# Performance work log

Measured on AMD Instinct MI355X. Metric: run time of the kernel, lower is better.

## Reference

```python
import jax, jax.numpy as jnp
import numpy as np

N = 1024
X_DIM = 128
Y_DIM = 128
HID = 256


def setup_inputs() -> dict:
    key = jax.random.key(0)
    ks = jax.random.split(key, 8)
    x_samples = jax.random.normal(ks[0], (N, X_DIM), dtype=jnp.float32)
    y_samples = jax.random.normal(ks[1], (N, Y_DIM), dtype=jnp.float32)
    # F_func: Linear(x_dim+y_dim -> hidden), ReLU, Linear(hidden -> 1)
    W1 = jax.random.normal(ks[2], (HID, X_DIM + Y_DIM), dtype=jnp.float32) * 0.05
    b1 = jax.random.normal(ks[3], (HID,), dtype=jnp.float32) * 0.05
    w2 = jax.random.normal(ks[4], (HID,), dtype=jnp.float32) * 0.05  # Linear(hidden,1) weight
    b2 = jax.random.normal(ks[5], (), dtype=jnp.float32) * 0.05
    # baseline: Linear(y_dim -> 1)
    wb = jax.random.normal(ks[6], (Y_DIM,), dtype=jnp.float32) * 0.05
    bb = jax.random.normal(ks[7], (), dtype=jnp.float32) * 0.05
    return {"x_samples": x_samples, "y_samples": y_samples,
            "W1": W1, "b1": b1, "w2": w2, "b2": b2, "wb": wb, "bb": bb}


def reference(x_samples, y_samples, W1, b1, w2, b2, wb, bb):
    n = y_samples.shape[0]
    # Split first linear: F(x,y) first layer = x @ Wx^T + y @ Wy^T + b1
    # (identical math to Linear on concat([x, y]))
    Wx = W1[:, :X_DIM]  # [H, x_dim]
    Wy = W1[:, X_DIM:]  # [H, y_dim]
    px = x_samples @ Wx.T  # [N, H]
    py = y_samples @ Wy.T  # [N, H]

    # T0: F on paired samples (x_i, y_i) -> [N]
    T0 = jax.nn.relu(px + py + b1) @ w2 + b2

    # T1[i, j] = F(x_j, y_i): x tiled over dim 0, y tiled over dim 1
    h = jax.nn.relu(px[None, :, :] + py[:, None, :] + b1)  # [N, N, H]
    T1 = h @ w2 + b2  # [N, N]

    # baseline log-scores on y -> [N]
    log_scores = y_samples @ wb + bb

    # (T1 - log_scores) broadcasts log_scores along dim 1 (the j/x axis),
    # matching torch's [N,N,1] - [N,1] broadcast; logsumexp over dim 1.
    lse = jax.scipy.special.logsumexp(T1 - log_scores[None, :], axis=1)  # [N]
    log_n = jnp.log(jnp.asarray(n, dtype=T1.dtype))
    lower_bound = (1.0 + T0.mean() - log_scores.mean()
                   - jnp.exp(lse - log_n).mean())
    return lower_bound
```

## Files before the change

kernel.cpp:

```cpp
#include <hip/hip_runtime.h>
#include <hip/hip_fp16.h>

#define NN 1024
#define HID 256
#define XD 128

typedef _Float16 h2 __attribute__((ext_vector_type(2)));
typedef _Float16 h8 __attribute__((ext_vector_type(8)));

#define WSF_BYTE_OFF 1049600
#define F_C    0
#define F_PART 1024
#define F_T0P  5120
#define F_LSP  5376

__device__ __forceinline__ h2 relu2(h2 x) {
  h2 z = {(_Float16)0, (_Float16)0};
  return __builtin_elementwise_max(x, z);
}

__device__ __forceinline__ float dot2f(h2 a, h2 b, float c) {
  return __builtin_amdgcn_fdot2(a, b, c, false);
}

__global__ __launch_bounds__(256) void prep_kernel(
    const float* __restrict__ x, const float* __restrict__ y,
    const float* __restrict__ W1, const float* __restrict__ b1,
    const float* __restrict__ w2, const float* __restrict__ b2p,
    const float* __restrict__ wb, const float* __restrict__ bbp,
    _Float16* __restrict__ wsh, float* __restrict__ wsf)
{
  __shared__ float sx[4][128];
  __shared__ float sy[4][128];
  __shared__ float st0[4][4];
  __shared__ float sls[4];
  const int t = threadIdx.x;
  const int blk = blockIdx.x;
  const int r0 = blk * 4;

  {
    const int rl = (t & 127) >> 5, f = t & 31;
    if (t < 128) {
      *(float4*)&sx[rl][f * 4] = *(const float4*)(x + (r0 + rl) * XD + f * 4);
    } else {
      *(float4*)&sy[rl][f * 4] = *(const float4*)(y + (r0 + rl) * XD + f * 4);
    }
  }
  __syncthreads();

  const int k = t;
  float apx[4] = {0,0,0,0};
  float apy[4] = {0,0,0,0};
  const float* wrow = W1 + k * 256;
  for (int dq = 0; dq < 32; ++dq) {
    float4 wx = *(const float4*)(wrow + dq * 4);
    float4 wy = *(const float4*)(wrow + 128 + dq * 4);
#pragma unroll
    for (int r = 0; r < 4; ++r) {
      float4 xv = *(const float4*)&sx[r][dq * 4];
      float4 yv = *(const float4*)&sy[r][dq * 4];
      apx[r] = fmaf(xv.x, wx.x, apx[r]);
      apx[r] = fmaf(xv.y, wx.y, apx[r]);
      apx[r] = fmaf(xv.z, wx.z, apx[r]);
      apx[r] = fmaf(xv.w, wx.w, apx[r]);
      apy[r] = fmaf(yv.x, wy.x, apy[r]);
      apy[r] = fmaf(yv.y, wy.y, apy[r]);
      apy[r] = fmaf(yv.z, wy.z, apy[r]);
      apy[r] = fmaf(yv.w, wy.w, apy[r]);
    }
  }
  const float b1k = b1[k];
#pragma unroll
  for (int r = 0; r < 4; ++r) apy[r] += b1k;

  {
    _Float16* pxh = wsh;
    _Float16* pyh = wsh + 262144;
    const int kq = k >> 6, q = (k >> 3) & 7, kl = k & 7;
#pragma unroll
    for (int r = 0; r < 4; ++r) {
      const int j = r0 + r;
      pxh[(j >> 6) * 16384 + kq * 4096 + q * 512 + (j & 63) * 8 + kl]
          = (_Float16)apx[r];
      pyh[j * 256 + k] = (_Float16)apy[r];
    }
  }

  const float w2k = w2[k];
  const float b2v = b2p[0];
  const int wv = t >> 6, lane = t & 63;
#pragma unroll
  for (int r = 0; r < 4; ++r) {
    float v = fmaxf(apx[r] + apy[r], 0.f) * w2k;
    for (int o = 32; o > 0; o >>= 1) v += __shfl_down(v, o);
    if (lane == 0) st0[wv][r] = v;
  }

  if (t < 128) {
    const int rl = t >> 5, f = t & 31;
    float p = 0.f;
#pragma unroll
    for (int l = 0; l < 4; ++l) p = fmaf(sy[rl][f * 4 + l], wb[f * 4 + l], p);
    for (int m = 16; m > 0; m >>= 1) p += __shfl_xor(p, m);
    if (f == 0) {
      const float lsv = p + bbp[0];
      sls[rl] = lsv;
      wsf[F_C + r0 + rl] = __expf(b2v - lsv);
    }
  }
  __syncthreads();
  if (t == 0) {
    float t0s = 0.f, lss = 0.f;
#pragma unroll
    for (int r = 0; r < 4; ++r) {
      t0s += st0[0][r] + st0[1][r] + st0[2][r] + st0[3][r] + b2v;
      lss += sls[r];
    }
    wsf[F_T0P + blk] = t0s;
    wsf[F_LSP + blk] = lss;
  }
  if (blk == 0 && t < 128) {
    h2 wv2;
    wv2.x = (_Float16)w2[2 * t];
    wv2.y = (_Float16)w2[2 * t + 1];
    ((h2*)(wsh + 524288))[t] = wv2;
  }
}

__global__ __launch_bounds__(256, 4) void main_kernel(
    const _Float16* __restrict__ wsh, float* __restrict__ wsf)
{
  __shared__ _Float16 spy[16 * 256];
  __shared__ _Float16 sw2[256];
  __shared__ float sComb[4][16][64];
  const int t = threadIdx.x;
  const int lane = t & 63;
  const int kq = t >> 6;
  const int blk = blockIdx.x;
  const int bj = blk & 15;
  const int i0 = (blk >> 4) * 16;

  h8 pxr[8];
  {
    const float4* gpx = (const float4*)(wsh + bj * 16384 + kq * 4096);
#pragma unroll
    for (int q = 0; q < 8; ++q) ((float4*)pxr)[q] = gpx[q * 64 + lane];
  }
  {
    const float4* gpy = (const float4*)(wsh + 262144 + (size_t)i0 * 256);
    ((float4*)spy)[t] = gpy[t];
    ((float4*)spy)[t + 256] = gpy[t + 256];
    if (t < 32) ((float4*)sw2)[t] = ((const float4*)(wsh + 524288))[t];
  }
  __syncthreads();

  h8 w2r[8];
#pragma unroll
  for (int q = 0; q < 8; ++q) w2r[q] = ((const h8*)(sw2 + kq * 64))[q];

  float acc[16];
#pragma unroll
  for (int ii = 0; ii < 16; ++ii) {
    const h8* prow = (const h8*)(spy + ii * 256 + kq * 64);
    float sa[4] = {0.f, 0.f, 0.f, 0.f};
#pragma unroll
    for (int q = 0; q < 8; ++q) {
      h8 pv = prow[q];
      const h2* p2 = (const h2*)&pv;
      const h2* x2 = (const h2*)&pxr[q];
      const h2* wp = (const h2*)&w2r[q];
      float s = sa[q & 3];
      s = dot2f(relu2(x2[0] + p2[0]), wp[0], s);
      s = dot2f(relu2(x2[1] + p2[1]), wp[1], s);
      s = dot2f(relu2(x2[2] + p2[2]), wp[2], s);
      s = dot2f(relu2(x2[3] + p2[3]), wp[3], s);
      sa[q & 3] = s;
    }
    acc[ii] = (sa[0] + sa[1]) + (sa[2] + sa[3]);
  }

#pragma unroll
  for (int ii = 0; ii < 16; ++ii) sComb[kq][ii][lane] = acc[ii];
  __syncthreads();

  const float cj = wsf[F_C + bj * 64 + lane];
  float ts = 0.f;
#pragma unroll
  for (int r = 0; r < 4; ++r) {
    const int ii = kq * 4 + r;
    float s = (sComb[0][ii][lane] + sComb[1][ii][lane])
            + (sComb[2][ii][lane] + sComb[3][ii][lane]);
    ts += __expf(s);
  }
  ts *= cj;
  for (int o = 32; o > 0; o >>= 1) ts += __shfl_down(ts, o);
  if (lane == 0) wsf[F_PART + blk * 4 + kq] = ts;
}

__global__ __launch_bounds__(256) void fin_kernel(
    const float* __restrict__ wsf, float* __restrict__ out)
{
  __shared__ float sr[4][3];
  const int t = threadIdx.x;
  float e = 0.f;
  const float4* pp = (const float4*)(wsf + F_PART);
#pragma unroll
  for (int s = 0; s < 4; ++s) {
    float4 ev = pp[t * 4 + s];
    e += (ev.x + ev.y) + (ev.z + ev.w);
  }
  float t0 = wsf[F_T0P + t];
  float ls = wsf[F_LSP + t];
  for (int o = 32; o > 0; o >>= 1) {
    e  += __shfl_down(e, o);
    t0 += __shfl_down(t0, o);
    ls += __shfl_down(ls, o);
  }
  if ((t & 63) == 0) {
    sr[t >> 6][0] = e;
    sr[t >> 6][1] = t0;
    sr[t >> 6][2] = ls;
  }
  __syncthreads();
  if (t == 0) {
    const float es  = sr[0][0] + sr[1][0] + sr[2][0] + sr[3][0];
    const float t0s = sr[0][1] + sr[1][1] + sr[2][1] + sr[3][1];
    const float lss = sr[0][2] + sr[1][2] + sr[2][2] + sr[3][2];
    out[0] = 1.0f + t0s * (1.0f / 1024.0f) - lss * (1.0f / 1024.0f)
                  - es * (1.0f / 1048576.0f);
  }
}

extern "C" void kernel_launch(void* const* d_in, const int* in_sizes, int n_in,
                              void* d_out, int out_size, void* d_ws, size_t ws_size,
                              hipStream_t stream) {
  const float* x  = (const float*)d_in[0];
  const float* y  = (const float*)d_in[1];
  const float* W1 = (const float*)d_in[2];
  const float* b1 = (const float*)d_in[3];
  const float* w2 = (const float*)d_in[4];
  const float* b2 = (const float*)d_in[5];
  const float* wb = (const float*)d_in[6];
  const float* bb = (const float*)d_in[7];
  _Float16* wsh = (_Float16*)d_ws;
  float* wsf = (float*)((char*)d_ws + WSF_BYTE_OFF);
  float* out = (float*)d_out;

  hipLaunchKernelGGL(prep_kernel, dim3(256), dim3(256), 0, stream,
                     x, y, W1, b1, w2, b2, wb, bb, wsh, wsf);
  hipLaunchKernelGGL(main_kernel, dim3(1024), dim3(256), 0, stream, wsh, wsf);
  hipLaunchKernelGGL(fin_kernel, dim3(1), dim3(256), 0, stream, wsf, out);
}
```

Before: 36.94 us.

## Widen main kernel tile to 128 x-columns with 8-way hidden split

Each main_kernel block now covers 16 y rows by 128 x columns with 512 threads, and each wave owns 32 hidden units for two 64-column groups. The px workspace layout is reordered to match. Each py value loaded into shared memory now serves twice as many columns, and the grid is halved to 512 blocks. The cost is a multi-stage tree reduction across 8 waves through shared memory with extra barriers, and the exp and epilogue work is concentrated in a single wave per block.

New measurement: 35.68 us. -3.4%, faster.

```diff
diff --git a/kernel.cpp b/kernel.cpp
--- a/kernel.cpp
+++ b/kernel.cpp
@@ -76,11 +76,12 @@
   {
     _Float16* pxh = wsh;
     _Float16* pyh = wsh + 262144;
-    const int kq = k >> 6, q = (k >> 3) & 7, kl = k & 7;
+    const int kg = k >> 5, ks = (k >> 3) & 3, kl = k & 7;
 #pragma unroll
     for (int r = 0; r < 4; ++r) {
       const int j = r0 + r;
-      pxh[(j >> 6) * 16384 + kq * 4096 + q * 512 + (j & 63) * 8 + kl]
+      const int jt = j >> 7, jj = (j >> 6) & 1, ln = j & 63;
+      pxh[((jt * 8 + kg) * 8 + ks * 2 + jj) * 512 + ln * 8 + kl]
           = (_Float16)apx[r];
       pyh[j * 256 + k] = (_Float16)apy[r];
     }
@@ -127,74 +128,113 @@
   }
 }
 
-__global__ __launch_bounds__(256, 4) void main_kernel(
+__global__ __launch_bounds__(512) void main_kernel(
     const _Float16* __restrict__ wsh, float* __restrict__ wsf)
 {
   __shared__ _Float16 spy[16 * 256];
   __shared__ _Float16 sw2[256];
-  __shared__ float sComb[4][16][64];
+  __shared__ float sComb[4][16][128];
   const int t = threadIdx.x;
   const int lane = t & 63;
-  const int kq = t >> 6;
+  const int kg = t >> 6;
   const int blk = blockIdx.x;
-  const int bj = blk & 15;
-  const int i0 = (blk >> 4) * 16;
+  const int bj = blk & 7;
+  const int i0 = (blk >> 3) * 16;
 
   h8 pxr[8];
   {
-    const float4* gpx = (const float4*)(wsh + bj * 16384 + kq * 4096);
-#pragma unroll
-    for (int q = 0; q < 8; ++q) ((float4*)pxr)[q] = gpx[q * 64 + lane];
+    const float4* gpx = (const float4*)wsh + ((bj * 8 + kg) * 8) * 64 + lane;
+#pragma unroll
+    for (int q = 0; q < 8; ++q) ((float4*)pxr)[q] = gpx[q * 64];
   }
   {
     const float4* gpy = (const float4*)(wsh + 262144 + (size_t)i0 * 256);
     ((float4*)spy)[t] = gpy[t];
-    ((float4*)spy)[t + 256] = gpy[t + 256];
     if (t < 32) ((float4*)sw2)[t] = ((const float4*)(wsh + 524288))[t];
   }
   __syncthreads();
 
-  h8 w2r[8];
-#pragma unroll
-  for (int q = 0; q < 8; ++q) w2r[q] = ((const h8*)(sw2 + kq * 64))[q];
-
-  float acc[16];
+  h8 w2r[4];
+#pragma unroll
+  for (int q = 0; q < 4; ++q) w2r[q] = ((const h8*)(sw2 + kg * 32))[q];
+
+  float acc[16][2];
+#pragma unroll
+  for (int ii = 0; ii < 16; ++ii) { acc[ii][0] = 0.f; acc[ii][1] = 0.f; }
+
 #pragma unroll
   for (int ii = 0; ii < 16; ++ii) {
-    const h8* prow = (const h8*)(spy + ii * 256 + kq * 64);
-    float sa[4] = {0.f, 0.f, 0.f, 0.f};
-#pragma unroll
-    for (int q = 0; q < 8; ++q) {
-      h8 pv = prow[q];
+    const h8* prow = (const h8*)(spy + ii * 256 + kg * 32);
+#pragma unroll
+    for (int ks = 0; ks < 4; ++ks) {
+      h8 pv = prow[ks];
       const h2* p2 = (const h2*)&pv;
-      const h2* x2 = (const h2*)&pxr[q];
-      const h2* wp = (const h2*)&w2r[q];
-      float s = sa[q & 3];
-      s = dot2f(relu2(x2[0] + p2[0]), wp[0], s);
-      s = dot2f(relu2(x2[1] + p2[1]), wp[1], s);
-      s = dot2f(relu2(x2[2] + p2[2]), wp[2], s);
-      s = dot2f(relu2(x2[3] + p2[3]), wp[3], s);
-      sa[q & 3] = s;
-    }
-    acc[ii] = (sa[0] + sa[1]) + (sa[2] + sa[3]);
-  }
-
-#pragma unroll
-  for (int ii = 0; ii < 16; ++ii) sComb[kq][ii][lane] = acc[ii];
-  __syncthreads();
-
-  const float cj = wsf[F_C + bj * 64 + lane];
-  float ts = 0.f;
-#pragma unroll
-  for (int r = 0; r < 4; ++r) {
-    const int ii = kq * 4 + r;
-    float s = (sComb[0][ii][lane] + sComb[1][ii][lane])
-            + (sComb[2][ii][lane] + sComb[3][ii][lane]);
-    ts += __expf(s);
-  }
-  ts *= cj;
-  for (int o = 32; o > 0; o >>= 1) ts += __shfl_down(ts, o);
-  if (lane == 0) wsf[F_PART + blk * 4 + kq] = ts;
+      const h2* wp = (const h2*)&w2r[ks];
+#pragma unroll
+      for (int jj = 0; jj < 2; ++jj) {
+        const h2* x2 = (const h2*)&pxr[ks * 2 + jj];
+        float s = acc[ii][jj];
+        s = dot2f(relu2(x2[0] + p2[0]), wp[0], s);
+        s = dot2f(relu2(x2[1] + p2[1]), wp[1], s);
+        s = dot2f(relu2(x2[2] + p2[2]), wp[2], s);
+        s = dot2f(relu2(x2[3] + p2[3]), wp[3], s);
+        acc[ii][jj] = s;
+      }
+    }
+  }
+
+  if (kg >= 4) {
+#pragma unroll
+    for (int ii = 0; ii < 16; ++ii) {
+      sComb[kg - 4][ii][lane]      = acc[ii][0];
+      sComb[kg - 4][ii][lane + 64] = acc[ii][1];
+    }
+  }
+  __syncthreads();
+  if (kg < 4) {
+#pragma unroll
+    for (int ii = 0; ii < 16; ++ii) {
+      acc[ii][0] += sComb[kg][ii][lane];
+      acc[ii][1] += sComb[kg][ii][lane + 64];
+    }
+  }
+  __syncthreads();
+  if (kg == 2 || kg == 3) {
+#pragma unroll
+    for (int ii = 0; ii < 16; ++ii) {
+      sComb[kg - 2][ii][lane]      = acc[ii][0];
+      sComb[kg - 2][ii][lane + 64] = acc[ii][1];
+    }
+  }
+  __syncthreads();
+  if (kg < 2) {
+#pragma unroll
+    for (int ii = 0; ii < 16; ++ii) {
+      acc[ii][0] += sComb[kg][ii][lane];
+      acc[ii][1] += sComb[kg][ii][lane + 64];
+    }
+  }
+  __syncthreads();
+  if (kg == 1) {
+#pragma unroll
+    for (int ii = 0; ii < 16; ++ii) {
+      sComb[0][ii][lane]      = acc[ii][0];
+      sComb[0][ii][lane + 64] = acc[ii][1];
+    }
+  }
+  __syncthreads();
+  if (kg == 0) {
+    const float* cbase = wsf + F_C + bj * 128;
+    const float c0 = cbase[lane], c1 = cbase[64 + lane];
+    float ts = 0.f;
+#pragma unroll
+    for (int ii = 0; ii < 16; ++ii) {
+      ts += __expf(acc[ii][0] + sComb[0][ii][lane]) * c0;
+      ts += __expf(acc[ii][1] + sComb[0][ii][lane + 64]) * c1;
+    }
+    for (int o = 32; o > 0; o >>= 1) ts += __shfl_down(ts, o);
+    if (lane == 0) wsf[F_PART + blk] = ts;
+  }
 }
 
 __global__ __launch_bounds__(256) void fin_kernel(
@@ -203,11 +243,9 @@
   __shared__ float sr[4][3];
   const int t = threadIdx.x;
   float e = 0.f;
-  const float4* pp = (const float4*)(wsf + F_PART);
-#pragma unroll
-  for (int s = 0; s < 4; ++s) {
-    float4 ev = pp[t * 4 + s];
-    e += (ev.x + ev.y) + (ev.z + ev.w);
+  if (t < 128) {
+    float4 ev = ((const float4*)(wsf + F_PART))[t];
+    e = (ev.x + ev.y) + (ev.z + ev.w);
   }
   float t0 = wsf[F_T0P + t];
   float ls = wsf[F_LSP + t];
@@ -248,6 +286,6 @@
 
   hipLaunchKernelGGL(prep_kernel, dim3(256), dim3(256), 0, stream,
                      x, y, W1, b1, w2, b2, wb, bb, wsh, wsf);
-  hipLaunchKernelGGL(main_kernel, dim3(1024), dim3(256), 0, stream, wsh, wsf);
+  hipLaunchKernelGGL(main_kernel, dim3(512), dim3(512), 0, stream, wsh, wsf);
   hipLaunchKernelGGL(fin_kernel, dim3(1), dim3(256), 0, stream, wsf, out);
 }
```
